# Kernel tuning notes

Hardware: AMD Instinct MI355X
Metric: run time of the kernel (lower is better)

Reference implementation:

```python
import jax, jax.numpy as jnp
import numpy as np

NUM_CLUSTERS = 1024
FEATURE_SIZE = 512
EPS_NORM = 1e-12   # torch F.normalize eps
EPS_P = 1e-16      # entropy clamp


def _l2_normalize(a):
    n = jnp.sqrt(jnp.sum(a * a, axis=-1, keepdims=True))
    return a / jnp.maximum(n, EPS_NORM)


def setup_inputs() -> dict:
    key = jax.random.key(0)
    kx, km = jax.random.split(key)
    x = jax.random.normal(kx, (65536, FEATURE_SIZE), dtype=jnp.float32)
    # cluster-center parameter (original uses SVD-orthonormal rows; any float
    # init is equivalent math-wise since rows are re-normalized in forward)
    m = jax.random.normal(km, (NUM_CLUSTERS, FEATURE_SIZE), dtype=jnp.float32)
    return {"x": x, "m": m}


def reference(x, m):
    # cosine-similarity logits: [N, K]
    y = jnp.einsum('nf,kf->nk', _l2_normalize(x), _l2_normalize(m))
    p = jax.nn.softmax(y, axis=-1)
    # clamp into (0, 1) exactly as the torch code does
    p = jnp.where(p <= 0, EPS_P, p)
    p = jnp.where(p >= 1, 1.0 - EPS_P, p)
    # shannon entropy per row, then mean
    ent = -jnp.sum(p * jnp.log(p), axis=-1)  # [N]
    intra = jnp.mean(ent)
    inter = jnp.float32(0.0)
    total = intra
    return (total, intra, inter)
```

## Files before the change

### kernel.cpp

```cpp
#include <hip/hip_runtime.h>
#include <hip/hip_bf16.h>

typedef float  f32x4  __attribute__((ext_vector_type(4)));
typedef unsigned long long u64;

#define N_ROWS 65536
#define N_F    512
#define N_CLU  1024

template <bool HI>
static __device__ __forceinline__ unsigned pk8(float a, float b, unsigned old) {
  return (unsigned)__builtin_amdgcn_cvt_pk_fp8_f32(a, b, (int)old, HI);
}

__global__ __launch_bounds__(256) void knorm_m(const float* __restrict__ m,
                                               u64* __restrict__ mnf) {
  const int wave = threadIdx.x >> 6, lane = threadIdx.x & 63;
  const int row = blockIdx.x * 4 + wave;
  const float* p = m + (size_t)row * N_F + lane * 8;
  float4 a = ((const float4*)p)[0];
  float4 b = ((const float4*)p)[1];
  float ss = a.x*a.x + a.y*a.y + a.z*a.z + a.w*a.w
           + b.x*b.x + b.y*b.y + b.z*b.z + b.w*b.w;
#pragma unroll
  for (int off = 1; off < 64; off <<= 1) ss += __shfl_xor(ss, off);
  const float inv = 1.0f / fmaxf(sqrtf(ss), 1e-12f);
  unsigned lo = pk8<false>(a.x*inv, a.y*inv, 0u);
  lo = pk8<true>(a.z*inv, a.w*inv, lo);
  unsigned hi = pk8<false>(b.x*inv, b.y*inv, 0u);
  hi = pk8<true>(b.z*inv, b.w*inv, hi);
  const u64 v = ((u64)hi << 32) | (u64)lo;
  const int i = lane >> 2, g = lane & 3;
  const int t = row >> 5, rb = (row >> 4) & 1, r16 = row & 15;
  mnf[((size_t)(t * 2 + rb) * 16 + i) * 64 + (r16 | (g << 4))] = v;
}

__global__ __launch_bounds__(512, 2) void kmain(const float* __restrict__ x,
                                                const u64* __restrict__ mnf,
                                                float* __restrict__ acc_out) {
  __shared__ __align__(16) u64 mbuf[2][32 * 64];
  const int tid = threadIdx.x, wave = tid >> 6, lane = tid & 63;
  const int rg = wave >> 1, ch = wave & 1;
  const int r16 = lane & 15, g = lane >> 4;

  long xb0[16], xb1[16];
  float L0 = 0.f, S0 = 0.f, L1 = 0.f, S1 = 0.f;

  auto loadset = [&](u64* s, int t) {
    const u64* p = mnf + (size_t)t * 2048 + tid;
#pragma unroll
    for (int q = 0; q < 4; ++q) s[q] = p[q * 512];
  };
  auto writeset = [&](const u64* s, int b) {
    u64* d = &mbuf[b][tid];
#pragma unroll
    for (int q = 0; q < 4; ++q) d[q * 512] = s[q];
  };

  u64 sA[4], sB[4];
  loadset(sA, 0);
  loadset(sB, 1);

  const int row0 = blockIdx.x * 128 + rg * 32;
  const float* px0 = x + (size_t)(row0 + r16) * N_F + g * 8;
  const float* px1 = x + (size_t)(row0 + 16 + r16) * N_F + g * 8;
  float ss0 = 0.f, ss1 = 0.f;
#pragma unroll
  for (int i = 0; i < 16; ++i) {
    float4 a = *(const float4*)(px0 + i * 32);
    float4 b = *(const float4*)(px0 + i * 32 + 4);
    ss0 += a.x*a.x + a.y*a.y + a.z*a.z + a.w*a.w
         + b.x*b.x + b.y*b.y + b.z*b.z + b.w*b.w;
    unsigned lo = pk8<false>(a.x, a.y, 0u);
    lo = pk8<true>(a.z, a.w, lo);
    unsigned hi = pk8<false>(b.x, b.y, 0u);
    hi = pk8<true>(b.z, b.w, hi);
    xb0[i] = (long)(((u64)hi << 32) | lo);
    float4 c = *(const float4*)(px1 + i * 32);
    float4 d = *(const float4*)(px1 + i * 32 + 4);
    ss1 += c.x*c.x + c.y*c.y + c.z*c.z + c.w*c.w
         + d.x*d.x + d.y*d.y + d.z*d.z + d.w*d.w;
    unsigned lo1 = pk8<false>(c.x, c.y, 0u);
    lo1 = pk8<true>(c.z, c.w, lo1);
    unsigned hi1 = pk8<false>(d.x, d.y, 0u);
    hi1 = pk8<true>(d.z, d.w, hi1);
    xb1[i] = (long)(((u64)hi1 << 32) | lo1);
  }
  ss0 += __shfl_xor(ss0, 16); ss0 += __shfl_xor(ss0, 32);
  ss1 += __shfl_xor(ss1, 16); ss1 += __shfl_xor(ss1, 32);
  const float inv0 = 1.0f / fmaxf(sqrtf(ss0), 1e-12f);
  const float inv1 = 1.0f / fmaxf(sqrtf(ss1), 1e-12f);

  auto tile = [&](int b) {
    const u64* mb = &mbuf[b][(size_t)ch * 1024 + lane];
    f32x4 a0 = {0.f,0.f,0.f,0.f}, a1 = {0.f,0.f,0.f,0.f};
#pragma unroll
    for (int i = 0; i < 16; ++i) {
      long af = (long)mb[i * 64];
      a0 = __builtin_amdgcn_mfma_f32_16x16x32_fp8_fp8(af, xb0[i], a0, 0, 0, 0);
      a1 = __builtin_amdgcn_mfma_f32_16x16x32_fp8_fp8(af, xb1[i], a1, 0, 0, 0);
    }
#pragma unroll
    for (int r = 0; r < 4; ++r) {
      { float y = a0[r] * inv0; float e = __expf(y); L0 += e; S0 = fmaf(e, y, S0); }
      { float y = a1[r] * inv1; float e = __expf(y); L1 += e; S1 = fmaf(e, y, S1); }
    }
  };

  writeset(sA, 0);
  loadset(sA, 2);
  asm volatile("s_waitcnt lgkmcnt(0)" ::: "memory");
  __builtin_amdgcn_s_barrier();

#pragma unroll 1
  for (int t = 0; t < 32; t += 2) {
    writeset(sB, 1);
    if (t + 3 < 32) loadset(sB, t + 3);
    tile(0);
    asm volatile("s_waitcnt lgkmcnt(0)" ::: "memory");
    __builtin_amdgcn_s_barrier();
    if (t + 2 < 32) writeset(sA, 0);
    if (t + 4 < 32) loadset(sA, t + 4);
    tile(1);
    asm volatile("s_waitcnt lgkmcnt(0)" ::: "memory");
    __builtin_amdgcn_s_barrier();
  }

  L0 += __shfl_xor(L0, 16); L0 += __shfl_xor(L0, 32);
  S0 += __shfl_xor(S0, 16); S0 += __shfl_xor(S0, 32);
  L1 += __shfl_xor(L1, 16); L1 += __shfl_xor(L1, 32);
  S1 += __shfl_xor(S1, 16); S1 += __shfl_xor(S1, 32);

  float* sc = (float*)&mbuf[0][0];
  const int rbase = rg * 32;
  if (lane < 16) {
    const int idx = ((rbase + r16) * 2 + ch) * 2;
    sc[idx] = L0; sc[idx + 1] = S0;
  } else if (lane < 32) {
    const int idx = ((rbase + 16 + (lane & 15)) * 2 + ch) * 2;
    sc[idx] = L1; sc[idx + 1] = S1;
  }
  __syncthreads();
  if (tid < 128) {
    const float L = sc[tid * 4 + 0] + sc[tid * 4 + 2];
    const float S = sc[tid * 4 + 1] + sc[tid * 4 + 3];
    float h = __logf(L) - S / L;
#pragma unroll
    for (int off = 1; off < 64; off <<= 1) h += __shfl_xor(h, off);
    if (lane == 0) atomicAdd(acc_out, h);
  }
}

__global__ void kfin(const float* __restrict__ acc, float* __restrict__ out) {
  const float mean = acc[0] * (1.0f / (float)N_ROWS);
  out[0] = mean;
  out[1] = mean;
  out[2] = 0.0f;
}

extern "C" void kernel_launch(void* const* d_in, const int* in_sizes, int n_in,
                              void* d_out, int out_size, void* d_ws, size_t ws_size,
                              hipStream_t stream) {
  const float* x = (const float*)d_in[0];
  const float* m = (const float*)d_in[1];
  float* acc = (float*)d_ws;
  u64* mnf = (u64*)((char*)d_ws + 64);

  (void)hipMemsetAsync(d_ws, 0, 64, stream);
  knorm_m<<<256, 256, 0, stream>>>(m, mnf);
  kmain<<<512, 512, 0, stream>>>(x, mnf, acc);
  kfin<<<1, 1, 0, stream>>>(acc, (float*)d_out);
}
```

Before: 112.6 us.

## Restructure main kernel: direct global-to-LDS staging, per-wave full cluster tiles, smaller blocks

Cluster-center tiles are now staged straight into LDS with global_load_lds instead of going through registers and ds_write. Each wave now owns 16 rows and computes both 16-cluster halves of each tile itself, so the cross-wave LDS reduction goes away. Blocks shrink to 256 threads with 64 rows, doubling the grid. The aim is to cut register staging, remove the final shared-memory combine and raise occupancy. The cost is that each M tile in LDS is reused by fewer rows, so LDS and L2 traffic per unit of work goes up.

Result: faster. 108.6 us (-3.6%).

```diff
diff --git a/kernel.cpp b/kernel.cpp
--- a/kernel.cpp
+++ b/kernel.cpp
@@ -11,6 +11,12 @@
 template <bool HI>
 static __device__ __forceinline__ unsigned pk8(float a, float b, unsigned old) {
   return (unsigned)__builtin_amdgcn_cvt_pk_fp8_f32(a, b, (int)old, HI);
+}
+
+__device__ __forceinline__ void gload_lds16(const void* g, void* l) {
+  __builtin_amdgcn_global_load_lds(
+      (const __attribute__((address_space(1))) void*)g,
+      (__attribute__((address_space(3))) void*)l, 16, 0, 0);
 }
 
 __global__ __launch_bounds__(256) void knorm_m(const float* __restrict__ m,
@@ -35,120 +41,77 @@
   mnf[((size_t)(t * 2 + rb) * 16 + i) * 64 + (r16 | (g << 4))] = v;
 }
 
-__global__ __launch_bounds__(512, 2) void kmain(const float* __restrict__ x,
+__global__ __launch_bounds__(256, 4) void kmain(const float* __restrict__ x,
                                                 const u64* __restrict__ mnf,
                                                 float* __restrict__ acc_out) {
-  __shared__ __align__(16) u64 mbuf[2][32 * 64];
+  __shared__ __align__(16) char mbuf[2][16384];
   const int tid = threadIdx.x, wave = tid >> 6, lane = tid & 63;
-  const int rg = wave >> 1, ch = wave & 1;
   const int r16 = lane & 15, g = lane >> 4;
 
-  long xb0[16], xb1[16];
-  float L0 = 0.f, S0 = 0.f, L1 = 0.f, S1 = 0.f;
-
-  auto loadset = [&](u64* s, int t) {
-    const u64* p = mnf + (size_t)t * 2048 + tid;
+  auto stage = [&](int t, int b) {
+    const char* gp = (const char*)mnf + (size_t)t * 16384 + wave * 1024 + lane * 16;
+    char* lp = &mbuf[b][wave * 1024];
 #pragma unroll
-    for (int q = 0; q < 4; ++q) s[q] = p[q * 512];
-  };
-  auto writeset = [&](const u64* s, int b) {
-    u64* d = &mbuf[b][tid];
-#pragma unroll
-    for (int q = 0; q < 4; ++q) d[q * 512] = s[q];
+    for (int q = 0; q < 4; ++q)
+      gload_lds16(gp + q * 4096, lp + q * 4096);
   };
 
-  u64 sA[4], sB[4];
-  loadset(sA, 0);
-  loadset(sB, 1);
+  stage(0, 0);
+  stage(1, 1);
 
-  const int row0 = blockIdx.x * 128 + rg * 32;
-  const float* px0 = x + (size_t)(row0 + r16) * N_F + g * 8;
-  const float* px1 = x + (size_t)(row0 + 16 + r16) * N_F + g * 8;
-  float ss0 = 0.f, ss1 = 0.f;
+  long xb[16];
+  const int row0 = blockIdx.x * 64 + wave * 16;
+  const float* px = x + (size_t)(row0 + r16) * N_F + g * 8;
+  float ss = 0.f;
 #pragma unroll
   for (int i = 0; i < 16; ++i) {
-    float4 a = *(const float4*)(px0 + i * 32);
-    float4 b = *(const float4*)(px0 + i * 32 + 4);
-    ss0 += a.x*a.x + a.y*a.y + a.z*a.z + a.w*a.w
-         + b.x*b.x + b.y*b.y + b.z*b.z + b.w*b.w;
+    float4 a = *(const float4*)(px + i * 32);
+    float4 b = *(const float4*)(px + i * 32 + 4);
+    ss += a.x*a.x + a.y*a.y + a.z*a.z + a.w*a.w
+        + b.x*b.x + b.y*b.y + b.z*b.z + b.w*b.w;
     unsigned lo = pk8<false>(a.x, a.y, 0u);
     lo = pk8<true>(a.z, a.w, lo);
     unsigned hi = pk8<false>(b.x, b.y, 0u);
     hi = pk8<true>(b.z, b.w, hi);
-    xb0[i] = (long)(((u64)hi << 32) | lo);
-    float4 c = *(const float4*)(px1 + i * 32);
-    float4 d = *(const float4*)(px1 + i * 32 + 4);
-    ss1 += c.x*c.x + c.y*c.y + c.z*c.z + c.w*c.w
-         + d.x*d.x + d.y*d.y + d.z*d.z + d.w*d.w;
-    unsigned lo1 = pk8<false>(c.x, c.y, 0u);
-    lo1 = pk8<true>(c.z, c.w, lo1);
-    unsigned hi1 = pk8<false>(d.x, d.y, 0u);
-    hi1 = pk8<true>(d.z, d.w, hi1);
-    xb1[i] = (long)(((u64)hi1 << 32) | lo1);
+    xb[i] = (long)(((u64)hi << 32) | lo);
   }
-  ss0 += __shfl_xor(ss0, 16); ss0 += __shfl_xor(ss0, 32);
-  ss1 += __shfl_xor(ss1, 16); ss1 += __shfl_xor(ss1, 32);
-  const float inv0 = 1.0f / fmaxf(sqrtf(ss0), 1e-12f);
-  const float inv1 = 1.0f / fmaxf(sqrtf(ss1), 1e-12f);
+  ss += __shfl_xor(ss, 16); ss += __shfl_xor(ss, 32);
+  const float inv = 1.0f / fmaxf(sqrtf(ss), 1e-12f);
 
-  auto tile = [&](int b) {
-    const u64* mb = &mbuf[b][(size_t)ch * 1024 + lane];
+  float L = 0.f, S = 0.f;
+
+  asm volatile("s_waitcnt vmcnt(4)" ::: "memory");
+  __builtin_amdgcn_s_barrier();
+
+#pragma unroll 1
+  for (int t = 0; t < 32; ++t) {
+    const int b = t & 1;
+    if (t + 1 < 32) stage(t + 1, b ^ 1);
+
+    const char* mb = &mbuf[b][lane * 8];
     f32x4 a0 = {0.f,0.f,0.f,0.f}, a1 = {0.f,0.f,0.f,0.f};
 #pragma unroll
     for (int i = 0; i < 16; ++i) {
-      long af = (long)mb[i * 64];
-      a0 = __builtin_amdgcn_mfma_f32_16x16x32_fp8_fp8(af, xb0[i], a0, 0, 0, 0);
-      a1 = __builtin_amdgcn_mfma_f32_16x16x32_fp8_fp8(af, xb1[i], a1, 0, 0, 0);
+      long f0 = *(const long*)(mb + i * 512);
+      long f1 = *(const long*)(mb + 8192 + i * 512);
+      a0 = __builtin_amdgcn_mfma_f32_16x16x32_fp8_fp8(f0, xb[i], a0, 0, 0, 0);
+      a1 = __builtin_amdgcn_mfma_f32_16x16x32_fp8_fp8(f1, xb[i], a1, 0, 0, 0);
     }
 #pragma unroll
     for (int r = 0; r < 4; ++r) {
-      { float y = a0[r] * inv0; float e = __expf(y); L0 += e; S0 = fmaf(e, y, S0); }
-      { float y = a1[r] * inv1; float e = __expf(y); L1 += e; S1 = fmaf(e, y, S1); }
+      { float y = a0[r] * inv; float e = __expf(y); L += e; S = fmaf(e, y, S); }
+      { float y = a1[r] * inv; float e = __expf(y); L += e; S = fmaf(e, y, S); }
     }
-  };
-
-  writeset(sA, 0);
-  loadset(sA, 2);
-  asm volatile("s_waitcnt lgkmcnt(0)" ::: "memory");
-  __builtin_amdgcn_s_barrier();
-
-#pragma unroll 1
-  for (int t = 0; t < 32; t += 2) {
-    writeset(sB, 1);
-    if (t + 3 < 32) loadset(sB, t + 3);
-    tile(0);
-    asm volatile("s_waitcnt lgkmcnt(0)" ::: "memory");
-    __builtin_amdgcn_s_barrier();
-    if (t + 2 < 32) writeset(sA, 0);
-    if (t + 4 < 32) loadset(sA, t + 4);
-    tile(1);
-    asm volatile("s_waitcnt lgkmcnt(0)" ::: "memory");
+    asm volatile("s_waitcnt vmcnt(0)" ::: "memory");
     __builtin_amdgcn_s_barrier();
   }
 
-  L0 += __shfl_xor(L0, 16); L0 += __shfl_xor(L0, 32);
-  S0 += __shfl_xor(S0, 16); S0 += __shfl_xor(S0, 32);
-  L1 += __shfl_xor(L1, 16); L1 += __shfl_xor(L1, 32);
-  S1 += __shfl_xor(S1, 16); S1 += __shfl_xor(S1, 32);
-
-  float* sc = (float*)&mbuf[0][0];
-  const int rbase = rg * 32;
-  if (lane < 16) {
-    const int idx = ((rbase + r16) * 2 + ch) * 2;
-    sc[idx] = L0; sc[idx + 1] = S0;
-  } else if (lane < 32) {
-    const int idx = ((rbase + 16 + (lane & 15)) * 2 + ch) * 2;
-    sc[idx] = L1; sc[idx + 1] = S1;
-  }
-  __syncthreads();
-  if (tid < 128) {
-    const float L = sc[tid * 4 + 0] + sc[tid * 4 + 2];
-    const float S = sc[tid * 4 + 1] + sc[tid * 4 + 3];
-    float h = __logf(L) - S / L;
+  L += __shfl_xor(L, 16); L += __shfl_xor(L, 32);
+  S += __shfl_xor(S, 16); S += __shfl_xor(S, 32);
+  float h = 0.25f * (__logf(L) - S / L);
 #pragma unroll
-    for (int off = 1; off < 64; off <<= 1) h += __shfl_xor(h, off);
-    if (lane == 0) atomicAdd(acc_out, h);
-  }
+  for (int off = 1; off < 64; off <<= 1) h += __shfl_xor(h, off);
+  if (lane == 0) atomicAdd(acc_out, h);
 }
 
 __global__ void kfin(const float* __restrict__ acc, float* __restrict__ out) {
@@ -168,6 +131,6 @@
 
   (void)hipMemsetAsync(d_ws, 0, 64, stream);
   knorm_m<<<256, 256, 0, stream>>>(m, mnf);
-  kmain<<<512, 512, 0, stream>>>(x, mnf, acc);
+  kmain<<<1024, 256, 0, stream>>>(x, mnf, acc);
   kfin<<<1, 1, 0, stream>>>(acc, (float*)d_out);
 }
```
